# Optimization experiments

Hardware: AMD Instinct MI355X
Metric: run time of the kernel (lower is better)

Reference implementation:

```python
import jax, jax.numpy as jnp
import numpy as np

B, N_PATTS, D_PATTS, L_PATTS, L_SEQ = 32, 32, 12, 32, 1024
L_OUT = 32
RHO = 1.0
BIG = 1e30  # stands in for +inf at DP boundaries (finite to keep grads clean)


def setup_inputs() -> dict:
    key = jax.random.key(0)
    kx, kp = jax.random.split(key)
    x = jax.random.normal(kx, (B, D_PATTS, L_SEQ), dtype=jnp.float32)
    patts = jax.random.normal(kp, (N_PATTS, D_PATTS, L_PATTS), dtype=jnp.float32)
    return {"x": x, "patts": patts}


def _pairwise_sqdist(x, patts):
    # cost[b,n,i,j] = sum_d (patts[n,d,i] - x[b,d,j])^2, shape [B,N,P,L]
    x2 = jnp.sum(x * x, axis=1)            # [B,L]
    p2 = jnp.sum(patts * patts, axis=1)    # [N,P]
    cross = jnp.einsum('bdl,ndp->bnpl', x, patts)  # [B,N,P,L]
    return p2[None, :, :, None] + x2[:, None, None, :] - 2.0 * cross


def _dp_column(a, c, w):
    # Solve cur[i] = c[i] + min(a[i], w*cur[i-1]) sequentially over pattern axis.
    # a, c: [B,N,P]; returns [B,N,P]
    a_t = jnp.moveaxis(a, -1, 0)  # [P,B,N]
    c_t = jnp.moveaxis(c, -1, 0)

    def step(cur_prev, ac):
        a_i, c_i = ac
        cur = c_i + jnp.minimum(a_i, w * cur_prev)
        return cur, cur

    init = jnp.full(c.shape[:-1], BIG, c.dtype)  # no row above the first
    _, cur = jax.lax.scan(step, init, (a_t, c_t))
    return jnp.moveaxis(cur, 0, -1)


def _dtw_dp(cost, w):
    # Weighted DTW recurrence:
    #   D[i,j] = cost[i,j] + min(D[i-1,j-1], w*D[i-1,j], w*D[i,j-1])
    # with D[0,0] = cost[0,0] and out-of-range predecessors = +inf.
    # cost: [B,N,P,L] -> D: [B,N,P,L]
    Bb, Nn, P, L = cost.shape
    cost_t = jnp.moveaxis(cost, -1, 0)  # [L,B,N,P]

    # first column j=0: D[i,0] = c[i,0] + w*D[i-1,0], D[0,0] = c[0,0]
    a0 = jnp.where(jnp.arange(P) == 0, 0.0, BIG).astype(cost.dtype)
    a0 = jnp.broadcast_to(a0, cost.shape[:3])
    d0 = _dp_column(a0, cost_t[0], w)  # [B,N,P]

    def outer_step(d_prev, c_col):
        # prev_shift[i] = D[i-1, j-1]; boundary row is +inf for j >= 1
        top = jnp.full_like(d_prev[..., :1], BIG)
        prev_shift = jnp.concatenate([top, d_prev[..., :-1]], axis=-1)
        a = jnp.minimum(prev_shift, w * d_prev)
        cur = _dp_column(a, c_col, w)
        return cur, cur

    _, rest = jax.lax.scan(outer_step, d0, cost_t[1:])  # [L-1,B,N,P]
    D = jnp.concatenate([d0[None], rest], axis=0)       # [L,B,N,P]
    return jnp.moveaxis(D, 0, -1)                       # [B,N,P,L]


def reference(x, patts):
    w = RHO ** (1.0 / L_PATTS)
    cost = _pairwise_sqdist(x, patts)   # [B,N,P,L]
    D = _dtw_dp(cost, w)                # [B,N,P,L]
    return D[..., -L_OUT:]              # [B,N,P,L_OUT]
```

## Files before the change

### kernel.cpp

```cpp
#include <hip/hip_runtime.h>


#define BIGF 1e30f
#define LL   1024
#define LOUT 32

using v4f = __attribute__((ext_vector_type(4))) float;

template<int CTRL>
__device__ __forceinline__ float dpp_self(float v) {
    return __int_as_float(__builtin_amdgcn_update_dpp(
        __float_as_int(v), __float_as_int(v), CTRL, 0xF, 0xF, false));
}
__device__ __forceinline__ float wshr1z(float v) {
    return __int_as_float(__builtin_amdgcn_update_dpp(
        0, __float_as_int(v), 0x138 , 0xF, 0xF, false));
}
__device__ __forceinline__ float rdlane(float v, int l) {
    return __int_as_float(__builtin_amdgcn_readlane(__float_as_int(v), l));
}

__device__ __forceinline__ float scan_min64_fast(float t, int lane) {
    t = fminf(t, dpp_self<0x111>(t));
    t = fminf(t, dpp_self<0x112>(t));
    t = fminf(t, dpp_self<0x114>(t));
    t = fminf(t, dpp_self<0x118>(t));
    float r0 = rdlane(t, 15), r1 = rdlane(t, 31), r2 = rdlane(t, 47);
    t = fminf(t, (lane >= 16) ? r0 : BIGF);
    t = fminf(t, (lane >= 32) ? r1 : BIGF);
    t = fminf(t, (lane >= 48) ? r2 : BIGF);
    return t;
}

__device__ __forceinline__ float scan_add64(float t, int lane) {
#pragma unroll
    for (int d = 1; d < 64; d <<= 1) {
        float o = __shfl_up(t, (unsigned)d, 64);
        t += (lane >= d) ? o : 0.0f;
    }
    return t;
}

__global__ __launch_bounds__(64, 1)
void dtw_kernel(const float* __restrict__ x, const float* __restrict__ patts,
                float* __restrict__ out) {
    __shared__ float pT[32 * 12];
    __shared__ float p2s[32];

    const int lane = threadIdx.x;
    const bool l0  = (lane == 0);
    const int blk  = blockIdx.x;
    const int b    = blk >> 5, n = blk & 31;
    const float* __restrict__ xb = x + b * (12 * LL);
    const float* __restrict__ pn = patts + n * (12 * 32);

    if (lane < 32) {
        float s2 = 0.f;
#pragma unroll
        for (int d = 0; d < 12; ++d) {
            float v = pn[d * 32 + lane];
            s2 = fmaf(v, v, s2);
            pT[lane * 12 + d] = -2.0f * v;
        }
        p2s[lane] = s2;
    }

    float SX[12][16];
#pragma unroll
    for (int d = 0; d < 12; ++d) {
#pragma unroll
        for (int c = 0; c < 4; ++c) {
            v4f v = *(const v4f*)(xb + d * LL + 16 * lane + 4 * c);
            SX[d][4*c+0] = v.x; SX[d][4*c+1] = v.y;
            SX[d][4*c+2] = v.z; SX[d][4*c+3] = v.w;
        }
    }
    float SX2[16];
#pragma unroll
    for (int k = 0; k < 16; ++k) {
        float a = 0.f;
#pragma unroll
        for (int d = 0; d < 12; ++d) a = fmaf(SX[d][k], SX[d][k], a);
        SX2[k] = a;
    }
#pragma unroll
    for (int d = 0; d < 12; ++d) {
#pragma unroll
        for (int k = 1; k < 16; ++k) SX[d][k] += SX[d][k-1];
        float tot = SX[d][15];
        float ex  = scan_add64(tot, lane) - tot;
#pragma unroll
        for (int k = 0; k < 16; ++k) SX[d][k] += ex;
    }
    {
#pragma unroll
        for (int k = 1; k < 16; ++k) SX2[k] += SX2[k-1];
        float tot = SX2[15];
        float ex  = scan_add64(tot, lane) - tot;
#pragma unroll
        for (int k = 0; k < 16; ++k) SX2[k] += ex;
    }
    float jp1[16];
#pragma unroll
    for (int k = 0; k < 16; ++k) jp1[k] = (float)(16 * lane + k + 1);

    __syncthreads();

    float pv[12], p2u;
#pragma unroll
    for (int d = 0; d < 12; ++d) pv[d] = pT[d];
    p2u = p2s[0];

    float S[16], Dp[16];
#pragma unroll
    for (int k = 0; k < 16; ++k) S[k] = fmaf(p2u, jp1[k], SX2[k]);
#pragma unroll
    for (int d = 0; d < 12; ++d)
#pragma unroll
        for (int k = 0; k < 16; ++k) S[k] = fmaf(pv[d], SX[d][k], S[k]);
#pragma unroll
    for (int k = 0; k < 16; ++k) Dp[k] = S[k];
    if (lane >= 62) {
        float* ob = out + blk * (32 * LOUT) + (lane - 62) * 16;
#pragma unroll
        for (int c = 0; c < 4; ++c) {
            v4f v = {Dp[4*c], Dp[4*c+1], Dp[4*c+2], Dp[4*c+3]};
            *(v4f*)(ob + 4 * c) = v;
        }
    }

#pragma unroll
    for (int d = 0; d < 12; ++d) pv[d] = pT[12 + d];
    p2u = p2s[1];
#pragma unroll
    for (int k = 0; k < 16; ++k) S[k] = fmaf(p2u, jp1[k], SX2[k]);
#pragma unroll
    for (int d = 0; d < 12; ++d)
#pragma unroll
        for (int k = 0; k < 16; ++k) S[k] = fmaf(pv[d], SX[d][k], S[k]);

#pragma unroll 1
    for (int i = 1; i < 32; ++i) {
        const int ip = (i + 1 < 32) ? i + 1 : 31;
        float pvn[12];
#pragma unroll
        for (int d = 0; d < 12; ++d) pvn[d] = pT[ip * 12 + d];
        float p2n = p2s[ip];

        float dsh = wshr1z(Dp[15]); dsh = l0 ? BIGF : dsh;
        float se  = wshr1z(S[15]);

        float m[16];
        m[0] = fminf(dsh, Dp[0]) - se;
#pragma unroll
        for (int k = 1; k < 16; ++k)
            m[k] = fminf(m[k-1], fminf(Dp[k-1], Dp[k]) - S[k-1]);

        float t = scan_min64_fast(m[15], lane);

        float Sn[16];
#pragma unroll
        for (int k = 0; k < 16; ++k) Sn[k] = fmaf(p2n, jp1[k], SX2[k]);
#pragma unroll
        for (int d = 0; d < 12; ++d)
#pragma unroll
            for (int k = 0; k < 16; ++k) Sn[k] = fmaf(pvn[d], SX[d][k], Sn[k]);

        float te = wshr1z(t); te = l0 ? BIGF : te;
#pragma unroll
        for (int k = 0; k < 16; ++k) Dp[k] = S[k] + fminf(te, m[k]);

        if (lane >= 62) {
            float* ob = out + blk * (32 * LOUT) + (lane - 62) * 16;
#pragma unroll
            for (int c = 0; c < 4; ++c) {
                v4f v = {Dp[4*c], Dp[4*c+1], Dp[4*c+2], Dp[4*c+3]};
                *(v4f*)(ob + i * 32 + 4 * c) = v;
            }
        }
#pragma unroll
        for (int k = 0; k < 16; ++k) S[k] = Sn[k];
    }
}

extern "C" void kernel_launch(void* const* d_in, const int* in_sizes, int n_in,
                              void* d_out, int out_size, void* d_ws, size_t ws_size,
                              hipStream_t stream) {
    const float* x     = (const float*)d_in[0];
    const float* patts = (const float*)d_in[1];
    float* out         = (float*)d_out;
    dtw_kernel<<<dim3(1024), dim3(64), 0, stream>>>(x, patts, out);
}
```

Measured before the change: 81.34 us.

## Split each DTW block's sequence across two waves with LDS boundary exchange

Each block now runs two wavefronts, each owning half of the 1024 sequence columns (8 per lane instead of 16). The row scan is done per wave, and wave 1 folds in wave 0's carry (last D, S and scan prefix) through shared memory with a barrier every row. The cost computation for the next row is no longer software-pipelined and is now computed inline. The aim is to halve the per-lane serial work and register pressure, at the price of a __syncthreads per pattern row and an extra cross-wave dependency.

```diff
diff --git a/kernel.cpp b/kernel.cpp
--- a/kernel.cpp
+++ b/kernel.cpp
@@ -31,7 +31,6 @@
     t = fminf(t, (lane >= 48) ? r2 : BIGF);
     return t;
 }
-
 __device__ __forceinline__ float scan_add64(float t, int lane) {
 #pragma unroll
     for (int d = 1; d < 64; d <<= 1) {
@@ -41,43 +40,47 @@
     return t;
 }
 
-__global__ __launch_bounds__(64, 1)
+__global__ __launch_bounds__(128)
+__attribute__((amdgpu_waves_per_eu(2, 2)))
 void dtw_kernel(const float* __restrict__ x, const float* __restrict__ patts,
                 float* __restrict__ out) {
     __shared__ float pT[32 * 12];
     __shared__ float p2s[32];
-
-    const int lane = threadIdx.x;
+    __shared__ float wtot[13];
+    __shared__ float bnd[2][3];
+
+    const int tid  = threadIdx.x;
+    const int wid  = tid >> 6;
+    const int lane = tid & 63;
     const bool l0  = (lane == 0);
     const int blk  = blockIdx.x;
     const int b    = blk >> 5, n = blk & 31;
     const float* __restrict__ xb = x + b * (12 * LL);
     const float* __restrict__ pn = patts + n * (12 * 32);
 
-    if (lane < 32) {
+    if (tid < 32) {
         float s2 = 0.f;
 #pragma unroll
         for (int d = 0; d < 12; ++d) {
-            float v = pn[d * 32 + lane];
+            float v = pn[d * 32 + tid];
             s2 = fmaf(v, v, s2);
-            pT[lane * 12 + d] = -2.0f * v;
-        }
-        p2s[lane] = s2;
-    }
-
-    float SX[12][16];
+            pT[tid * 12 + d] = -2.0f * v;
+        }
+        p2s[tid] = s2;
+    }
+
+    const int col0 = 512 * wid + 8 * lane;
+    float SX[12][8];
 #pragma unroll
     for (int d = 0; d < 12; ++d) {
-#pragma unroll
-        for (int c = 0; c < 4; ++c) {
-            v4f v = *(const v4f*)(xb + d * LL + 16 * lane + 4 * c);
-            SX[d][4*c+0] = v.x; SX[d][4*c+1] = v.y;
-            SX[d][4*c+2] = v.z; SX[d][4*c+3] = v.w;
-        }
-    }
-    float SX2[16];
-#pragma unroll
-    for (int k = 0; k < 16; ++k) {
+        v4f a = *(const v4f*)(xb + d * LL + col0);
+        v4f c = *(const v4f*)(xb + d * LL + col0 + 4);
+        SX[d][0] = a.x; SX[d][1] = a.y; SX[d][2] = a.z; SX[d][3] = a.w;
+        SX[d][4] = c.x; SX[d][5] = c.y; SX[d][6] = c.z; SX[d][7] = c.w;
+    }
+    float SX2[8];
+#pragma unroll
+    for (int k = 0; k < 8; ++k) {
         float a = 0.f;
 #pragma unroll
         for (int d = 0; d < 12; ++d) a = fmaf(SX[d][k], SX[d][k], a);
@@ -86,100 +89,118 @@
 #pragma unroll
     for (int d = 0; d < 12; ++d) {
 #pragma unroll
-        for (int k = 1; k < 16; ++k) SX[d][k] += SX[d][k-1];
-        float tot = SX[d][15];
-        float ex  = scan_add64(tot, lane) - tot;
-#pragma unroll
-        for (int k = 0; k < 16; ++k) SX[d][k] += ex;
+        for (int k = 1; k < 8; ++k) SX[d][k] += SX[d][k-1];
+        float tot  = SX[d][7];
+        float incl = scan_add64(tot, lane);
+        float ex   = incl - tot;
+#pragma unroll
+        for (int k = 0; k < 8; ++k) SX[d][k] += ex;
+        if (wid == 0 && lane == 63) wtot[d] = incl;
     }
     {
 #pragma unroll
-        for (int k = 1; k < 16; ++k) SX2[k] += SX2[k-1];
-        float tot = SX2[15];
-        float ex  = scan_add64(tot, lane) - tot;
-#pragma unroll
-        for (int k = 0; k < 16; ++k) SX2[k] += ex;
-    }
-    float jp1[16];
-#pragma unroll
-    for (int k = 0; k < 16; ++k) jp1[k] = (float)(16 * lane + k + 1);
-
+        for (int k = 1; k < 8; ++k) SX2[k] += SX2[k-1];
+        float tot  = SX2[7];
+        float incl = scan_add64(tot, lane);
+        float ex   = incl - tot;
+#pragma unroll
+        for (int k = 0; k < 8; ++k) SX2[k] += ex;
+        if (wid == 0 && lane == 63) wtot[12] = incl;
+    }
     __syncthreads();
-
-    float pv[12], p2u;
-#pragma unroll
-    for (int d = 0; d < 12; ++d) pv[d] = pT[d];
-    p2u = p2s[0];
-
-    float S[16], Dp[16];
-#pragma unroll
-    for (int k = 0; k < 16; ++k) S[k] = fmaf(p2u, jp1[k], SX2[k]);
-#pragma unroll
-    for (int d = 0; d < 12; ++d)
-#pragma unroll
-        for (int k = 0; k < 16; ++k) S[k] = fmaf(pv[d], SX[d][k], S[k]);
-#pragma unroll
-    for (int k = 0; k < 16; ++k) Dp[k] = S[k];
-    if (lane >= 62) {
-        float* ob = out + blk * (32 * LOUT) + (lane - 62) * 16;
-#pragma unroll
-        for (int c = 0; c < 4; ++c) {
-            v4f v = {Dp[4*c], Dp[4*c+1], Dp[4*c+2], Dp[4*c+3]};
-            *(v4f*)(ob + 4 * c) = v;
-        }
-    }
-
-#pragma unroll
-    for (int d = 0; d < 12; ++d) pv[d] = pT[12 + d];
-    p2u = p2s[1];
-#pragma unroll
-    for (int k = 0; k < 16; ++k) S[k] = fmaf(p2u, jp1[k], SX2[k]);
-#pragma unroll
-    for (int d = 0; d < 12; ++d)
-#pragma unroll
-        for (int k = 0; k < 16; ++k) S[k] = fmaf(pv[d], SX[d][k], S[k]);
+    if (wid == 1) {
+#pragma unroll
+        for (int d = 0; d < 12; ++d) {
+            float o = wtot[d];
+#pragma unroll
+            for (int k = 0; k < 8; ++k) SX[d][k] += o;
+        }
+        float o2 = wtot[12];
+#pragma unroll
+        for (int k = 0; k < 8; ++k) SX2[k] += o2;
+    }
+    float jp1[8];
+#pragma unroll
+    for (int k = 0; k < 8; ++k) jp1[k] = (float)(col0 + k + 1);
+
+    float* ob = out + blk * (32 * LOUT) + (col0 - (LL - LOUT));
+
+    float S[8], Dp[8];
+    {
+        float pv[12];
+#pragma unroll
+        for (int d = 0; d < 12; ++d) pv[d] = pT[d];
+        float p2u = p2s[0];
+#pragma unroll
+        for (int k = 0; k < 8; ++k) S[k] = fmaf(p2u, jp1[k], SX2[k]);
+#pragma unroll
+        for (int d = 0; d < 12; ++d)
+#pragma unroll
+            for (int k = 0; k < 8; ++k) S[k] = fmaf(pv[d], SX[d][k], S[k]);
+#pragma unroll
+        for (int k = 0; k < 8; ++k) Dp[k] = S[k];
+        if (wid == 1 && lane >= 60) {
+            v4f v0 = {Dp[0], Dp[1], Dp[2], Dp[3]};
+            v4f v1 = {Dp[4], Dp[5], Dp[6], Dp[7]};
+            *(v4f*)(ob + 0) = v0;
+            *(v4f*)(ob + 4) = v1;
+        }
+    }
 
 #pragma unroll 1
     for (int i = 1; i < 32; ++i) {
-        const int ip = (i + 1 < 32) ? i + 1 : 31;
-        float pvn[12];
-#pragma unroll
-        for (int d = 0; d < 12; ++d) pvn[d] = pT[ip * 12 + d];
-        float p2n = p2s[ip];
-
-        float dsh = wshr1z(Dp[15]); dsh = l0 ? BIGF : dsh;
-        float se  = wshr1z(S[15]);
-
-        float m[16];
-        m[0] = fminf(dsh, Dp[0]) - se;
-#pragma unroll
-        for (int k = 1; k < 16; ++k)
+        const int s = i & 1;
+        float dbv = rdlane(Dp[7], 63);
+
+        float pv[12];
+#pragma unroll
+        for (int d = 0; d < 12; ++d) pv[d] = pT[i * 12 + d];
+        float p2u = p2s[i];
+#pragma unroll
+        for (int k = 0; k < 8; ++k) S[k] = fmaf(p2u, jp1[k], SX2[k]);
+#pragma unroll
+        for (int d = 0; d < 12; ++d)
+#pragma unroll
+            for (int k = 0; k < 8; ++k) S[k] = fmaf(pv[d], SX[d][k], S[k]);
+
+        float dsh = wshr1z(Dp[7]);
+        float se  = wshr1z(S[7]);
+        float z0  = fminf(l0 ? BIGF : dsh, Dp[0]) - se;
+        if (wid == 1 && l0) z0 = BIGF;
+        float m[8];
+        m[0] = z0;
+#pragma unroll
+        for (int k = 1; k < 8; ++k)
             m[k] = fminf(m[k-1], fminf(Dp[k-1], Dp[k]) - S[k-1]);
 
-        float t = scan_min64_fast(m[15], lane);
-
-        float Sn[16];
-#pragma unroll
-        for (int k = 0; k < 16; ++k) Sn[k] = fmaf(p2n, jp1[k], SX2[k]);
-#pragma unroll
-        for (int d = 0; d < 12; ++d)
-#pragma unroll
-            for (int k = 0; k < 16; ++k) Sn[k] = fmaf(pvn[d], SX[d][k], Sn[k]);
-
-        float te = wshr1z(t); te = l0 ? BIGF : te;
-#pragma unroll
-        for (int k = 0; k < 16; ++k) Dp[k] = S[k] + fminf(te, m[k]);
-
-        if (lane >= 62) {
-            float* ob = out + blk * (32 * LOUT) + (lane - 62) * 16;
-#pragma unroll
-            for (int c = 0; c < 4; ++c) {
-                v4f v = {Dp[4*c], Dp[4*c+1], Dp[4*c+2], Dp[4*c+3]};
-                *(v4f*)(ob + i * 32 + 4 * c) = v;
-            }
-        }
-#pragma unroll
-        for (int k = 0; k < 16; ++k) S[k] = Sn[k];
+        float t   = scan_min64_fast(m[7], lane);
+        float te  = wshr1z(t); te = l0 ? BIGF : te;
+
+        if (wid == 0) {
+            float sbv = rdlane(S[7], 63);
+            float T0v = rdlane(t, 63);
+            if (l0) { bnd[s][0] = dbv; bnd[s][1] = sbv; bnd[s][2] = T0v; }
+        }
+        __syncthreads();
+
+        float B;
+        if (wid == 0) {
+            B = te;
+        } else {
+            float dsh_b = bnd[s][0], se_b = bnd[s][1], T0 = bnd[s][2];
+            float d0  = rdlane(Dp[0], 0);
+            float z0c = fminf(dsh_b, d0) - se_b;
+            B = fminf(fminf(T0, z0c), te);
+        }
+#pragma unroll
+        for (int k = 0; k < 8; ++k) Dp[k] = S[k] + fminf(B, m[k]);
+
+        if (wid == 1 && lane >= 60) {
+            v4f v0 = {Dp[0], Dp[1], Dp[2], Dp[3]};
+            v4f v1 = {Dp[4], Dp[5], Dp[6], Dp[7]};
+            *(v4f*)(ob + i * 32 + 0) = v0;
+            *(v4f*)(ob + i * 32 + 4) = v1;
+        }
     }
 }
 
@@ -189,5 +210,5 @@
     const float* x     = (const float*)d_in[0];
     const float* patts = (const float*)d_in[1];
     float* out         = (float*)d_out;
-    dtw_kernel<<<dim3(1024), dim3(64), 0, stream>>>(x, patts, out);
-}
+    dtw_kernel<<<dim3(1024), dim3(128), 0, stream>>>(x, patts, out);
+}
```

Result: slower. 84.30 us (+3.6%).
